# Kernel tuning notes

Measured on AMD Instinct MI355X. Metric: run time of the kernel, lower is better.

The kernel has to match this reference:

```python
import jax, jax.numpy as jnp
import numpy as np

N, IN_DIM, HID, OUT, NH = 512, 256, 256, 256, 4
HD = OUT // NH  # head_dim = 64
EPS = 1e-5


def _mlp(x, w1, b1, w2, b2):
    return jax.nn.relu(x @ w1 + b1) @ w2 + b2


def setup_inputs() -> dict:
    key = jax.random.key(0)
    ks = jax.random.split(key, 32)

    def rn(k, shape, fan_in):
        return (jax.random.normal(k, shape, jnp.float32) / np.float32(np.sqrt(fan_in)))

    V = jax.random.normal(ks[0], (N, IN_DIM), jnp.float32)
    adj = jax.random.randint(ks[1], (N, N), 0, 2, jnp.int32)
    adj = adj.at[jnp.arange(N), jnp.arange(N)].set(1)  # self-edges: avoid all -inf rows
    prev_hidden = jax.random.normal(ks[2], (N, HID), jnp.float32)
    z = jnp.zeros
    return dict(
        V=V, adj=adj, prev_hidden=prev_hidden,
        W1=rn(ks[3], (IN_DIM, HID), IN_DIM),
        a_std0=rn(ks[4], (HID, 1), HID), a_std1=rn(ks[5], (HID, 1), HID),
        ce_w1=rn(ks[6], (2 * IN_DIM, HID), 2 * IN_DIM), ce_b1=z((HID,), jnp.float32),
        ce_w2=rn(ks[7], (HID, HD), HID), ce_b2=z((HD,), jnp.float32),
        a_c0=rn(ks[8], (HD, 1), HD), a_c1=rn(ks[9], (HD, 1), HD),
        te_w1=rn(ks[10], (IN_DIM + HID, HID), IN_DIM + HID), te_b1=z((HID,), jnp.float32),
        te_w2=rn(ks[11], (HID, HD), HID), te_b2=z((HD,), jnp.float32),
        a_t0=rn(ks[12], (HD, 1), HD), a_t1=rn(ks[13], (HD, 1), HD),
        co_w1=rn(ks[14], (3 * IN_DIM, HID), 3 * IN_DIM), co_b1=z((HID,), jnp.float32),
        co_w2=rn(ks[15], (HID, HD), HID), co_b2=z((HD,), jnp.float32),
        a_co0=rn(ks[16], (HD, 1), HD), a_co1=rn(ks[17], (HD, 1), HD),
        W2=rn(ks[18], (HID + 2 * HD + 1, OUT), HID + 2 * HD + 1),
        Wo=rn(ks[19], (OUT, OUT), OUT), bo=z((OUT,), jnp.float32),
        ln_g=jnp.ones((OUT,), jnp.float32), ln_b=z((OUT,), jnp.float32),
    )


def reference(V, adj, prev_hidden, W1, a_std0, a_std1,
              ce_w1, ce_b1, ce_w2, ce_b2, a_c0, a_c1,
              te_w1, te_b1, te_w2, te_b2, a_t0, a_t1,
              co_w1, co_b1, co_w2, co_b2, a_co0, a_co1,
              W2, Wo, bo, ln_g, ln_b):
    ninf = -jnp.inf

    # ---- standard GAT branch -> H1: (N, HID) ----
    Wh1 = V @ W1
    s1 = Wh1 @ a_std0 + (Wh1 @ a_std1).T                      # (N, N)
    s1 = jnp.where(adj == 0, ninf, s1)
    H1 = jax.nn.softmax(s1, axis=1) @ Wh1

    # ---- causal branch: all ordered pairs i!=j, global softmax -> H2: (N, HD) ----
    pair = jnp.concatenate([jnp.broadcast_to(V[:, None, :], (N, N, IN_DIM)),
                            jnp.broadcast_to(V[None, :, :], (N, N, IN_DIM))], axis=-1)
    cf = _mlp(pair, ce_w1, ce_b1, ce_w2, ce_b2)               # (N, N, HD)
    cs = (cf @ (a_c0 + a_c1))[..., 0]                         # (N, N)
    cs = jnp.where(jnp.eye(N, dtype=bool), ninf, cs)          # exclude i==j pairs
    ca = jax.nn.softmax(cs.reshape(-1)).reshape(N, N, 1)
    H2 = jnp.broadcast_to((ca * cf).sum((0, 1)), (N, HD))

    # ---- temporal branch: (N,1) scores broadcast against causal mask -> running mean ----
    tf = _mlp(jnp.concatenate([V, prev_hidden], axis=-1), te_w1, te_b1, te_w2, te_b2)  # (N, HD)
    ts = tf @ (a_t0 + a_t1)                                   # (N, 1)
    cmask = jnp.triu(jnp.ones((N, N), bool), 1)
    tsb = jnp.where(cmask, ninf, jnp.broadcast_to(ts, (N, N)))
    H3 = jax.nn.softmax(tsb, axis=1) @ tf                     # (N, HD)

    # ---- coop branch: first two neighbors by index; size-1 softmax; buggy pad -> (N,1) ----
    order = jnp.argsort((1 - adj).astype(jnp.int32), axis=1, stable=True)  # adj==1 first, index order
    nb = V[order[:, :2]]                                      # (N, 2, IN_DIM)
    valid = ((adj == 1).sum(axis=1) >= 2)
    nb = jnp.where(valid[:, None, None], nb, jnp.zeros_like(nb))
    ci = jnp.concatenate([V, nb[:, 0], nb[:, 1]], axis=-1)    # (N, 3*IN_DIM)
    cf4 = _mlp(ci, co_w1, co_b1, co_w2, co_b2)                # (N, HD)
    ca4 = jax.nn.softmax(cf4 @ (a_co0 + a_co1), axis=1)       # (N,1): softmax over size-1 -> ones
    h4vec = (ca4.T @ cf4)[0]                                  # (HD,)
    # original: squeeze(-2)->(HD,), dim==1 -> unsqueeze(-1)->(HD,1), zero-pad rows to N
    H4 = jnp.zeros((N, 1), V.dtype).at[:HD, 0].set(h4vec)

    # ---- combine, lazy W2, proj, LN, ELU (dropout identity in eval) ----
    Hc = jnp.concatenate([H1, H2, H3, H4], axis=-1) @ W2      # (N, OUT)
    out = Hc @ Wo + bo
    mu = out.mean(-1, keepdims=True)
    var = ((out - mu) ** 2).mean(-1, keepdims=True)
    out = (out - mu) / jnp.sqrt(var + EPS) * ln_g + ln_b
    return jax.nn.elu(out)
```

## Files before the change

kernel.cpp:

```cpp
#include <hip/hip_runtime.h>
#include <math.h>

#define NN 512
#define HD 64
#define EPSV 1e-5f

struct GD {
  const float *A, *A2, *A3, *A4;
  const int* I;
  const float *B, *bias;
  float* C;
  int M, K, Nn, mode, act;
};

#define GEMM_SMEM (8704 + 17408 + 2176)
#define MEGA_SMEM 38656

__device__ __forceinline__ void gemm_body(char* smem, const GD& d, int bx, int by) {
  float (*At)[34] = (float (*)[34])smem;
  float (*Bs)[68] = (float (*)[68])(smem + 8704);
  char* extra = smem + 8704 + 17408;
  int* nbl = (int*)extra;
  float* wscl = (float*)extra;
  float* rowsuml = wscl + 512;

  const int t = threadIdx.x;
  const int tx = t & 15, ty = t >> 4;
  const int rowbase = by * 32, colbase = bx * 64;
  const int K = d.K, Nn = d.Nn, mode = d.mode, M = d.M;
  if (rowbase >= M) return;

  if (mode == 2) {
    int wave = t >> 6, lane = t & 63;
    for (int rr = wave; rr < 32; rr += 4) {
      int row = rowbase + rr;
      int n0 = -1, n1 = -1, cnt = 0;
      for (int c = 0; c < 8; ++c) {
        unsigned long long mm = __ballot(d.I[row * NN + c * 64 + lane] != 0);
        cnt += (int)__popcll(mm);
        if (n0 < 0 && mm) { n0 = c * 64 + (int)__builtin_ctzll(mm); mm &= mm - 1; }
        if (n1 < 0 && mm) { n1 = c * 64 + (int)__builtin_ctzll(mm); }
      }
      if (lane == 0) { nbl[rr * 3] = n0; nbl[rr * 3 + 1] = n1; nbl[rr * 3 + 2] = (cnt >= 2); }
    }
    __syncthreads();
  } else if (mode == 4) {
    wscl[t] = d.A2[t];
    wscl[256 + t] = d.A2[256 + t];
    __syncthreads();
  }

  float4 aR[2], bR[4];
  float rs0 = 0.f, rs1 = 0.f;

  auto loadA = [&](int k0) {
#pragma unroll
    for (int j = 0; j < 2; ++j) {
      int idx = t + j * 256;
      int r = idx >> 4, c0 = (idx & 15) * 4;
      int row = rowbase + r, gk = k0 + c0;
      float4 v4 = make_float4(0.f, 0.f, 0.f, 0.f);
      if (mode == 0) {
        if (row < M && gk < K) v4 = *(const float4*)&d.A[(size_t)row * K + gk];
      } else if (mode == 1) {
        if (gk < 256) v4 = *(const float4*)&d.A[row * 256 + gk];
        else v4 = *(const float4*)&d.A2[row * 256 + gk - 256];
      } else if (mode == 2) {
        int seg = gk >> 8;
        int src = (seg == 0) ? row : (nbl[r * 3 + 2] ? nbl[r * 3 + seg - 1] : -1);
        if (src >= 0) v4 = *(const float4*)&d.A[src * 256 + (gk & 255)];
      } else if (mode == 3) {
        if (gk + 3 < 256) v4 = *(const float4*)&d.A[row * 256 + gk];
        else if (gk >= 256 && gk + 3 < 320) v4 = *(const float4*)&d.A2[gk - 256];
        else if (gk >= 320 && gk + 3 < 384) v4 = *(const float4*)&d.A3[row * 64 + gk - 320];
        else if (gk == 384) v4.x = (row < 64) ? d.A4[row] : 0.f;
      } else {
        int4 a4 = *(const int4*)&d.I[row * NN + gk];
        v4.x = a4.x ? wscl[gk + 0] : 0.f;
        v4.y = a4.y ? wscl[gk + 1] : 0.f;
        v4.z = a4.z ? wscl[gk + 2] : 0.f;
        v4.w = a4.w ? wscl[gk + 3] : 0.f;
        float ss = v4.x + v4.y + v4.z + v4.w;
        if (j == 0) rs0 += ss; else rs1 += ss;
      }
      aR[j] = v4;
    }
  };
  auto loadB = [&](int k0) {
#pragma unroll
    for (int j = 0; j < 4; ++j) {
      int idx = t + j * 256;
      int r = idx >> 4, c0 = (idx & 15) * 4;
      int gk = k0 + r;
      float4 v4 = make_float4(0.f, 0.f, 0.f, 0.f);
      if (gk < K) v4 = *(const float4*)&d.B[(size_t)gk * Nn + colbase + c0];
      bR[j] = v4;
    }
  };
  auto stos = [&]() {
#pragma unroll
    for (int j = 0; j < 2; ++j) {
      int idx = t + j * 256;
      int r = idx >> 4, c0 = (idx & 15) * 4;
      At[c0 + 0][r] = aR[j].x;
      At[c0 + 1][r] = aR[j].y;
      At[c0 + 2][r] = aR[j].z;
      At[c0 + 3][r] = aR[j].w;
    }
#pragma unroll
    for (int j = 0; j < 4; ++j) {
      int idx = t + j * 256;
      int r = idx >> 4, c0 = (idx & 15) * 4;
      *(float4*)&Bs[r][c0] = bR[j];
    }
  };

  float4 acc0 = make_float4(0.f, 0.f, 0.f, 0.f);
  float4 acc1 = make_float4(0.f, 0.f, 0.f, 0.f);

  int iters = (K + 63) >> 6;
  loadA(0); loadB(0);
  for (int it = 0; it < iters; ++it) {
    stos();
    __syncthreads();
    if (it + 1 < iters) { loadA((it + 1) << 6); loadB((it + 1) << 6); }
#pragma unroll 8
    for (int kk = 0; kk < 64; ++kk) {
      float2 a = *(const float2*)&At[kk][ty * 2];
      float4 b = *(const float4*)&Bs[kk][tx * 4];
      acc0.x += a.x * b.x; acc0.y += a.x * b.y; acc0.z += a.x * b.z; acc0.w += a.x * b.w;
      acc1.x += a.y * b.x; acc1.y += a.y * b.y; acc1.z += a.y * b.z; acc1.w += a.y * b.w;
    }
    __syncthreads();
  }

  if (mode == 4) {
    float a0 = rs0, a1 = rs1;
#pragma unroll
    for (int off = 8; off; off >>= 1) {
      a0 += __shfl_xor(a0, off, 16);
      a1 += __shfl_xor(a1, off, 16);
    }
    if ((t & 15) == 0) { rowsuml[t >> 4] = a0; rowsuml[16 + (t >> 4)] = a1; }
    __syncthreads();
  }

  int col = colbase + tx * 4;
  float4 bv = make_float4(0.f, 0.f, 0.f, 0.f);
  if (d.bias) bv = *(const float4*)&d.bias[col];
  int row0 = rowbase + ty * 2;
  float4 o0, o1;
  o0.x = acc0.x + bv.x; o0.y = acc0.y + bv.y; o0.z = acc0.z + bv.z; o0.w = acc0.w + bv.w;
  o1.x = acc1.x + bv.x; o1.y = acc1.y + bv.y; o1.z = acc1.z + bv.z; o1.w = acc1.w + bv.w;
  if (d.act) {
    o0.x = fmaxf(o0.x, 0.f); o0.y = fmaxf(o0.y, 0.f); o0.z = fmaxf(o0.z, 0.f); o0.w = fmaxf(o0.w, 0.f);
    o1.x = fmaxf(o1.x, 0.f); o1.y = fmaxf(o1.y, 0.f); o1.z = fmaxf(o1.z, 0.f); o1.w = fmaxf(o1.w, 0.f);
  }
  if (mode == 4) {
    float s0 = 1.f / rowsuml[ty * 2], s1 = 1.f / rowsuml[ty * 2 + 1];
    o0.x *= s0; o0.y *= s0; o0.z *= s0; o0.w *= s0;
    o1.x *= s1; o1.y *= s1; o1.z *= s1; o1.w *= s1;
  }
  if (row0 < M)     *(float4*)&d.C[(size_t)row0 * Nn + col] = o0;
  if (row0 + 1 < M) *(float4*)&d.C[(size_t)(row0 + 1) * Nn + col] = o1;
}

__device__ void wsc_body(char* smem, const float* W1, const float* a_std1,
                         const float* V, float* expwsc, int grp) {
  float* asl = (float*)smem;
  float* ul  = asl + 256;
  int t = threadIdx.x;
  asl[t] = a_std1[t];
  __syncthreads();
  {
    float s = 0.f;
    const float* wr = W1 + t * 256;
    for (int h = 0; h < 256; h += 4) {
      float4 w4 = *(const float4*)&wr[h];
      float4 a4 = *(const float4*)&asl[h];
      s += w4.x * a4.x + w4.y * a4.y + w4.z * a4.z + w4.w * a4.w;
    }
    ul[t] = s;
  }
  __syncthreads();
  int wave = t >> 6, lane = t & 63;
  float4 u4 = *(const float4*)&ul[lane * 4];
  int j0 = grp * 128;
  for (int j = j0 + wave; j < j0 + 128; j += 4) {
    float4 v4 = *(const float4*)&V[j * 256 + lane * 4];
    float s = v4.x * u4.x + v4.y * u4.y + v4.z * u4.z + v4.w * u4.w;
#pragma unroll
    for (int off = 32; off; off >>= 1) s += __shfl_xor(s, off, 64);
    if (lane == 0) expwsc[j] = __expf(s);
  }
}

struct GD7 { GD d[7]; };
__global__ __launch_bounds__(256) void gemm7_k(GD7 ds) {
  __shared__ __align__(16) char smem[GEMM_SMEM];
  int z = blockIdx.z;
  if (z == 6) {
    if (blockIdx.y != 0) return;
    wsc_body(smem, ds.d[6].A, ds.d[6].A2, ds.d[6].A3, ds.d[6].C, blockIdx.x);
    return;
  }
  gemm_body(smem, ds.d[z], blockIdx.x, blockIdx.y);
}
__global__ __launch_bounds__(256) void gemm1_k(GD d) {
  __shared__ __align__(16) char smem[GEMM_SMEM];
  gemm_body(smem, d, blockIdx.x, blockIdx.y);
}

__device__ void pair_body(char* smem,
    const float* __restrict__ P, const float* __restrict__ Q,
    const float* __restrict__ b1, const float* __restrict__ ce_w2,
    const float* __restrict__ a_c0, const float* __restrict__ a_c1,
    float* __restrict__ mpart, float* __restrict__ dpart,
    float* __restrict__ spart, int byy, int bxx) {
  float* Pl  = (float*)smem;
  float* Ql  = Pl + 16 * 260;
  float* el  = Ql + 16 * 260;
  float* wcl = el + 16 * 20;
  float* red = wcl + 256;
  float* sk  = red + 256;
  float* sbl = sk + 256;
  int t = threadIdx.x;

  if (t < 64) red[t] = a_c0[t] + a_c1[t];
  __syncthreads();
  {
    float s = 0.f;
    const float* w2r = ce_w2 + t * 64;
#pragma unroll 8
    for (int h = 0; h < 64; ++h) s += w2r[h] * red[h];
    wcl[t] = s;
  }
  int i0 = byy * 16, j0 = bxx * 16;
  for (int e = t; e < 1024; e += 256) {
    int r = e >> 6, c4 = (e & 63) * 4;
    float4 bb = *(const float4*)&b1[c4];
    float4 pv = *(const float4*)&P[(i0 + r) * 256 + c4];
    pv.x += bb.x; pv.y += bb.y; pv.z += bb.z; pv.w += bb.w;
    *(float4*)&Pl[r * 260 + c4] = pv;
    *(float4*)&Ql[r * 260 + c4] = *(const float4*)&Q[(j0 + r) * 256 + c4];
  }
  __syncthreads();

  int a = t >> 4, b = t & 15;
  const float* pr = &Pl[a * 260];
  const float* qr = &Ql[b * 260];
  float4 c4a = make_float4(0.f, 0.f, 0.f, 0.f);
#pragma unroll 8
  for (int k4 = 0; k4 < 64; ++k4) {
    float4 w = *(const float4*)&wcl[k4 * 4];
    float4 p = *(const float4*)&pr[k4 * 4];
    float4 q = *(const float4*)&qr[k4 * 4];
    c4a.x += fmaxf(p.x + q.x, 0.f) * w.x;
    c4a.y += fmaxf(p.y + q.y, 0.f) * w.y;
    c4a.z += fmaxf(p.z + q.z, 0.f) * w.z;
    c4a.w += fmaxf(p.w + q.w, 0.f) * w.w;
  }
  float s = c4a.x + c4a.y + c4a.z + c4a.w;
  if (i0 + a == j0 + b) s = -INFINITY;
  red[t] = s; __syncthreads();
  for (int ss = 128; ss; ss >>= 1) { if (t < ss) red[t] = fmaxf(red[t], red[t + ss]); __syncthreads(); }
  float mb = red[0];
  __syncthreads();
  float e = __expf(s - mb);
  el[a * 20 + b] = e;
  red[t] = e; __syncthreads();
  for (int ss = 128; ss; ss >>= 1) { if (t < ss) red[t] += red[t + ss]; __syncthreads(); }
  float db = red[0];
  __syncthreads();

  float qv[16];
#pragma unroll
  for (int j = 0; j < 16; ++j) qv[j] = Ql[j * 260 + t];
  float rk = 0.f;
#pragma unroll 4
  for (int i = 0; i < 16; ++i) {
    float pv = Pl[i * 260 + t];
    const float* erow = &el[i * 20];
#pragma unroll
    for (int j4 = 0; j4 < 4; ++j4) {
      float4 e4 = *(const float4*)&erow[j4 * 4];
      rk += e4.x * fmaxf(pv + qv[j4 * 4 + 0], 0.f);
      rk += e4.y * fmaxf(pv + qv[j4 * 4 + 1], 0.f);
      rk += e4.z * fmaxf(pv + qv[j4 * 4 + 2], 0.f);
      rk += e4.w * fmaxf(pv + qv[j4 * 4 + 3], 0.f);
    }
  }
  sk[t] = rk;
  __syncthreads();
  {
    int h = t & 63, q = t >> 6;
    float s2 = 0.f;
    for (int k = q * 64; k < q * 64 + 64; ++k) s2 += sk[k] * ce_w2[k * 64 + h];
    sbl[q * 64 + h] = s2;
  }
  __syncthreads();
  int blk = byy * 32 + bxx;
  if (t < 64) spart[blk * 64 + t] = sbl[t] + sbl[64 + t] + sbl[128 + t] + sbl[192 + t];
  if (t == 0) { mpart[blk] = mb; dpart[blk] = db; }
}

struct MegaArgs {
  const float *P, *Q, *b1, *ce_w2, *a_c0, *a_c1;
  float *mpart, *dpart, *spart;
  GD gH1, gTf, gCf;
};

__global__ __launch_bounds__(256) void mega_k(MegaArgs a) {
  __shared__ __align__(16) char smem[MEGA_SMEM];
  int b = blockIdx.x;
  if (b < 64) {
    gemm_body(smem, a.gH1, b & 3, b >> 2);
  } else if (b < 80) {
    gemm_body(smem, a.gTf, 0, b - 64);
  } else if (b < 96) {
    gemm_body(smem, a.gCf, 0, b - 80);
  } else {
    int p = b - 96;
    pair_body(smem, a.P, a.Q, a.b1, a.ce_w2, a.a_c0, a.a_c1,
              a.mpart, a.dpart, a.spart, p >> 5, p & 31);
  }
}

__global__ __launch_bounds__(1024) void mini_k(
    const float* __restrict__ mpart, const float* __restrict__ dpart,
    const float* __restrict__ spart, const float* __restrict__ ce_b2,
    float* __restrict__ H2row,
    const float* __restrict__ tf, float* __restrict__ H3,
    const float* __restrict__ cf4, float* __restrict__ h4vec) {
  __shared__ float A[1024];
  __shared__ float Bsh[1024];
  __shared__ float segsum[16][65];
  int b = blockIdx.x, t = threadIdx.x;
  if (b == 0) {
    float mv = mpart[t];
    A[t] = mv; __syncthreads();
    for (int s = 512; s; s >>= 1) { if (t < s) A[t] = fmaxf(A[t], A[t + s]); __syncthreads(); }
    float M = A[0];
    __syncthreads();
    float e = __expf(mv - M);
    Bsh[t] = e;
    A[t] = e * dpart[t];
    __syncthreads();
    for (int s = 512; s; s >>= 1) { if (t < s) A[t] += A[t + s]; __syncthreads(); }
    float D = A[0];
    __syncthreads();
    int h = t & 63, g = t >> 6;
    float s2 = 0.f;
    for (int b2 = g * 64; b2 < g * 64 + 64; ++b2) s2 += Bsh[b2] * spart[b2 * 64 + h];
    A[t] = s2;
    __syncthreads();
    for (int p = 8; p; p >>= 1) { if (g < p) A[g * 64 + h] += A[(g + p) * 64 + h]; __syncthreads(); }
    if (t < 64) H2row[t] = A[t] / D + ce_b2[t];
  } else if (b == 1) {
    int h = t & 63, g = t >> 6;
    float vals[32];
    float run = 0.f;
#pragma unroll
    for (int r = 0; r < 32; ++r) { run += tf[(g * 32 + r) * 64 + h]; vals[r] = run; }
    segsum[g][h] = run;
    __syncthreads();
    float off = 0.f;
    for (int gg = 0; gg < g; ++gg) off += segsum[gg][h];
#pragma unroll
    for (int r = 0; r < 32; ++r) {
      int i = g * 32 + r;
      H3[i * 64 + h] = (vals[r] + off) / (float)(i + 1);
    }
  } else {
    int h = t & 63, g = t >> 6;
    float s = 0.f;
    for (int r = 0; r < 32; ++r) s += cf4[(g * 32 + r) * 64 + h];
    A[g * 64 + h] = s;
    __syncthreads();
    for (int p = 8; p; p >>= 1) { if (g < p) A[g * 64 + h] += A[(g + p) * 64 + h]; __syncthreads(); }
    if (t < 64) h4vec[t] = A[t];
  }
}

__global__ void ln_elu_kernel(const float* __restrict__ X, const float* __restrict__ g,
                              const float* __restrict__ b, float* __restrict__ out) {
  __shared__ float red[256];
  int i = blockIdx.x, tid = threadIdx.x;
  float x = X[i * 256 + tid];
  red[tid] = x; __syncthreads();
  for (int s = 128; s; s >>= 1) { if (tid < s) red[tid] += red[tid + s]; __syncthreads(); }
  float mu = red[0] * (1.f / 256.f);
  __syncthreads();
  float d = x - mu;
  red[tid] = d * d; __syncthreads();
  for (int s = 128; s; s >>= 1) { if (tid < s) red[tid] += red[tid + s]; __syncthreads(); }
  float var = red[0] * (1.f / 256.f);
  float y = d / sqrtf(var + EPSV) * g[tid] + b[tid];
  out[i * 256 + tid] = (y > 0.f) ? y : (expf(y) - 1.f);
}

static GD mkgd(const float* A, const float* A2, const float* A3, const float* A4,
               const int* I, const float* B, const float* bias, float* C,
               int M, int K, int Nn, int mode, int act) {
  GD g{A, A2, A3, A4, I, B, bias, C, M, K, Nn, mode, act};
  return g;
}

extern "C" void kernel_launch(void* const* d_in, const int* in_sizes, int n_in,
                              void* d_out, int out_size, void* d_ws, size_t ws_size,
                              hipStream_t stream) {
  const float* V      = (const float*)d_in[0];
  const int*   adj    = (const int*)  d_in[1];
  const float* ph     = (const float*)d_in[2];
  const float* W1     = (const float*)d_in[3];
  const float* a_std1 = (const float*)d_in[5];
  const float* ce_w1  = (const float*)d_in[6];
  const float* ce_b1  = (const float*)d_in[7];
  const float* ce_w2  = (const float*)d_in[8];
  const float* ce_b2  = (const float*)d_in[9];
  const float* a_c0   = (const float*)d_in[10];
  const float* a_c1   = (const float*)d_in[11];
  const float* te_w1  = (const float*)d_in[12];
  const float* te_b1  = (const float*)d_in[13];
  const float* te_w2  = (const float*)d_in[14];
  const float* te_b2  = (const float*)d_in[15];
  const float* co_w1  = (const float*)d_in[18];
  const float* co_b1  = (const float*)d_in[19];
  const float* co_w2  = (const float*)d_in[20];
  const float* co_b2  = (const float*)d_in[21];
  const float* W2     = (const float*)d_in[24];
  const float* Wo     = (const float*)d_in[25];
  const float* bo     = (const float*)d_in[26];
  const float* ln_g   = (const float*)d_in[27];
  const float* ln_b   = (const float*)d_in[28];
  float* out = (float*)d_out;

  float* ws = (float*)d_ws;
  size_t off = 0;
  auto alloc = [&](size_t n) { float* p = ws + off; off += (n + 15) & ~(size_t)15; return p; };

  float* Wh1    = alloc(512 * 256);
  float* Pb     = alloc(512 * 256);
  float* Qb     = alloc(512 * 256);
  float* tfh    = alloc(512 * 256);
  float* cf4h   = alloc(512 * 256);
  float* H1     = alloc(512 * 256);
  float* Wfused = alloc(385 * 256);
  float* T2     = alloc(512 * 256);
  float* tf     = alloc(512 * 64);
  float* cf4    = alloc(512 * 64);
  float* H3     = alloc(512 * 64);
  float* spart  = alloc(1024 * 64);
  float* mpart  = alloc(1024);
  float* dpart  = alloc(1024);
  float* expwsc = alloc(512);
  float* H2row  = alloc(64);
  float* h4vec  = alloc(64);
  (void)ws_size; (void)in_sizes; (void)n_in; (void)out_size;

  GD7 sA;
  sA.d[0] = mkgd(V, 0, 0, 0, 0, W1, 0, Wh1, 512, 256, 256, 0, 0);
  sA.d[1] = mkgd(V, 0, 0, 0, 0, ce_w1, 0, Pb, 512, 256, 256, 0, 0);
  sA.d[2] = mkgd(V, 0, 0, 0, 0, ce_w1 + 256 * 256, 0, Qb, 512, 256, 256, 0, 0);
  sA.d[3] = mkgd(V, ph, 0, 0, 0, te_w1, te_b1, tfh, 512, 512, 256, 1, 1);
  sA.d[4] = mkgd(V, 0, 0, 0, adj, co_w1, co_b1, cf4h, 512, 768, 256, 2, 1);
  sA.d[5] = mkgd(W2, 0, 0, 0, 0, Wo, 0, Wfused, 385, 256, 256, 0, 0);
  sA.d[6] = mkgd(W1, a_std1, V, 0, 0, 0, 0, expwsc, 512, 256, 1, 6, 0);
  gemm7_k<<<dim3(4, 16, 7), 256, 0, stream>>>(sA);

  MegaArgs ma;
  ma.P = Pb; ma.Q = Qb; ma.b1 = ce_b1; ma.ce_w2 = ce_w2;
  ma.a_c0 = a_c0; ma.a_c1 = a_c1;
  ma.mpart = mpart; ma.dpart = dpart; ma.spart = spart;
  ma.gH1 = mkgd(0, expwsc, 0, 0, adj, Wh1, 0, H1, 512, 512, 256, 4, 0);
  ma.gTf = mkgd(tfh, 0, 0, 0, 0, te_w2, te_b2, tf, 512, 256, 64, 0, 0);
  ma.gCf = mkgd(cf4h, 0, 0, 0, 0, co_w2, co_b2, cf4, 512, 256, 64, 0, 0);
  mega_k<<<1120, 256, 0, stream>>>(ma);

  mini_k<<<3, 1024, 0, stream>>>(mpart, dpart, spart, ce_b2, H2row, tf, H3, cf4, h4vec);

  GD gF = mkgd(H1, H2row, H3, h4vec, 0, Wfused, bo, T2, 512, 385, 256, 3, 0);
  gemm1_k<<<dim3(4, 16), 256, 0, stream>>>(gF);

  ln_elu_kernel<<<512, 256, 0, stream>>>(T2, ln_g, ln_b, out);
}
```

Baseline: 201.8 us.

## Use split-bf16 MFMA (3-pass) for the tiled GEMM instead of FP32 FMAs

Replaces the scalar FP32 inner product in the shared GEMM body with MFMA 16x16x32 bf16 instructions. Each float operand is split into high and low bf16 halves, and three MFMA passes (hh, hl, lh) approximate FP32 accuracy. The shared-memory layout changes to bf16 high/low tiles, with B transposed. The epilogue is remapped to the MFMA output layout, which writes scalars instead of float4. The aim is to cut ALU time in the matmuls, at the cost of extra split work, scalar stores, and slightly lower precision.

```diff
diff --git a/kernel.cpp b/kernel.cpp
--- a/kernel.cpp
+++ b/kernel.cpp
@@ -4,6 +4,11 @@
 #define NN 512
 #define HD 64
 #define EPSV 1e-5f
+
+typedef unsigned short u16;
+typedef short s4v __attribute__((ext_vector_type(4)));
+typedef short s8v __attribute__((ext_vector_type(8)));
+typedef float f4v __attribute__((ext_vector_type(4)));
 
 struct GD {
   const float *A, *A2, *A3, *A4;
@@ -13,19 +18,27 @@
   int M, K, Nn, mode, act;
 };
 
-#define GEMM_SMEM (8704 + 17408 + 2176)
+#define GEMM_SMEM 28800
 #define MEGA_SMEM 38656
 
+__device__ __forceinline__ void split_bf16(float x, u16& h, u16& l) {
+  unsigned xb = __float_as_uint(x);
+  float hf = __uint_as_float(xb & 0xffff0000u);
+  h = (u16)(xb >> 16);
+  l = (u16)(__float_as_uint(x - hf) >> 16);
+}
+
 __device__ __forceinline__ void gemm_body(char* smem, const GD& d, int bx, int by) {
-  float (*At)[34] = (float (*)[34])smem;
-  float (*Bs)[68] = (float (*)[68])(smem + 8704);
-  char* extra = smem + 8704 + 17408;
+  u16 (*Ah)[72] = (u16(*)[72])smem;
+  u16 (*Al)[72] = (u16(*)[72])(smem + 4608);
+  u16 (*Bh)[68] = (u16(*)[68])(smem + 9216);
+  u16 (*Bl)[68] = (u16(*)[68])(smem + 9216 + 8704);
+  char* extra = smem + 26624;
   int* nbl = (int*)extra;
   float* wscl = (float*)extra;
   float* rowsuml = wscl + 512;
 
   const int t = threadIdx.x;
-  const int tx = t & 15, ty = t >> 4;
   const int rowbase = by * 32, colbase = bx * 64;
   const int K = d.K, Nn = d.Nn, mode = d.mode, M = d.M;
   if (rowbase >= M) return;
@@ -102,21 +115,34 @@
     for (int j = 0; j < 2; ++j) {
       int idx = t + j * 256;
       int r = idx >> 4, c0 = (idx & 15) * 4;
-      At[c0 + 0][r] = aR[j].x;
-      At[c0 + 1][r] = aR[j].y;
-      At[c0 + 2][r] = aR[j].z;
-      At[c0 + 3][r] = aR[j].w;
+      float v[4] = {aR[j].x, aR[j].y, aR[j].z, aR[j].w};
+      u16 h[4], l[4];
+#pragma unroll
+      for (int e = 0; e < 4; ++e) split_bf16(v[e], h[e], l[e]);
+      *(short4*)&Ah[r][c0] = make_short4(h[0], h[1], h[2], h[3]);
+      *(short4*)&Al[r][c0] = make_short4(l[0], l[1], l[2], l[3]);
     }
 #pragma unroll
     for (int j = 0; j < 4; ++j) {
       int idx = t + j * 256;
       int r = idx >> 4, c0 = (idx & 15) * 4;
-      *(float4*)&Bs[r][c0] = bR[j];
+      float v[4] = {bR[j].x, bR[j].y, bR[j].z, bR[j].w};
+#pragma unroll
+      for (int e = 0; e < 4; ++e) {
+        u16 h, l;
+        split_bf16(v[e], h, l);
+        Bh[c0 + e][r] = h;
+        Bl[c0 + e][r] = l;
+      }
     }
   };
 
-  float4 acc0 = make_float4(0.f, 0.f, 0.f, 0.f);
-  float4 acc1 = make_float4(0.f, 0.f, 0.f, 0.f);
+  f4v acc0 = {0.f, 0.f, 0.f, 0.f};
+  f4v acc1 = {0.f, 0.f, 0.f, 0.f};
+
+  const int w4 = t >> 6;
+  const int lrow = t & 15;
+  const int lk = ((t & 63) >> 4) * 8;
 
   int iters = (K + 63) >> 6;
   loadA(0); loadB(0);
@@ -124,12 +150,31 @@
     stos();
     __syncthreads();
     if (it + 1 < iters) { loadA((it + 1) << 6); loadB((it + 1) << 6); }
-#pragma unroll 8
-    for (int kk = 0; kk < 64; ++kk) {
-      float2 a = *(const float2*)&At[kk][ty * 2];
-      float4 b = *(const float4*)&Bs[kk][tx * 4];
-      acc0.x += a.x * b.x; acc0.y += a.x * b.y; acc0.z += a.x * b.z; acc0.w += a.x * b.w;
-      acc1.x += a.y * b.x; acc1.y += a.y * b.y; acc1.z += a.y * b.z; acc1.w += a.y * b.w;
+    const u16* bhrow = Bh[w4 * 16 + lrow];
+    const u16* blrow = Bl[w4 * 16 + lrow];
+#pragma unroll
+    for (int ks = 0; ks < 2; ++ks) {
+      int ko = ks * 32 + lk;
+      s4v bh_0 = *(const s4v*)&bhrow[ko];
+      s4v bh_1 = *(const s4v*)&bhrow[ko + 4];
+      s4v bl_0 = *(const s4v*)&blrow[ko];
+      s4v bl_1 = *(const s4v*)&blrow[ko + 4];
+      s8v bh = __builtin_shufflevector(bh_0, bh_1, 0, 1, 2, 3, 4, 5, 6, 7);
+      s8v bl = __builtin_shufflevector(bl_0, bl_1, 0, 1, 2, 3, 4, 5, 6, 7);
+      {
+        s8v ah = *(const s8v*)&Ah[lrow][ko];
+        s8v al = *(const s8v*)&Al[lrow][ko];
+        acc0 = __builtin_amdgcn_mfma_f32_16x16x32_bf16(ah, bh, acc0, 0, 0, 0);
+        acc0 = __builtin_amdgcn_mfma_f32_16x16x32_bf16(ah, bl, acc0, 0, 0, 0);
+        acc0 = __builtin_amdgcn_mfma_f32_16x16x32_bf16(al, bh, acc0, 0, 0, 0);
+      }
+      {
+        s8v ah = *(const s8v*)&Ah[16 + lrow][ko];
+        s8v al = *(const s8v*)&Al[16 + lrow][ko];
+        acc1 = __builtin_amdgcn_mfma_f32_16x16x32_bf16(ah, bh, acc1, 0, 0, 0);
+        acc1 = __builtin_amdgcn_mfma_f32_16x16x32_bf16(ah, bl, acc1, 0, 0, 0);
+        acc1 = __builtin_amdgcn_mfma_f32_16x16x32_bf16(al, bh, acc1, 0, 0, 0);
+      }
     }
     __syncthreads();
   }
@@ -145,24 +190,22 @@
     __syncthreads();
   }
 
-  int col = colbase + tx * 4;
-  float4 bv = make_float4(0.f, 0.f, 0.f, 0.f);
-  if (d.bias) bv = *(const float4*)&d.bias[col];
-  int row0 = rowbase + ty * 2;
-  float4 o0, o1;
-  o0.x = acc0.x + bv.x; o0.y = acc0.y + bv.y; o0.z = acc0.z + bv.z; o0.w = acc0.w + bv.w;
-  o1.x = acc1.x + bv.x; o1.y = acc1.y + bv.y; o1.z = acc1.z + bv.z; o1.w = acc1.w + bv.w;
-  if (d.act) {
-    o0.x = fmaxf(o0.x, 0.f); o0.y = fmaxf(o0.y, 0.f); o0.z = fmaxf(o0.z, 0.f); o0.w = fmaxf(o0.w, 0.f);
-    o1.x = fmaxf(o1.x, 0.f); o1.y = fmaxf(o1.y, 0.f); o1.z = fmaxf(o1.z, 0.f); o1.w = fmaxf(o1.w, 0.f);
-  }
-  if (mode == 4) {
-    float s0 = 1.f / rowsuml[ty * 2], s1 = 1.f / rowsuml[ty * 2 + 1];
-    o0.x *= s0; o0.y *= s0; o0.z *= s0; o0.w *= s0;
-    o1.x *= s1; o1.y *= s1; o1.z *= s1; o1.w *= s1;
-  }
-  if (row0 < M)     *(float4*)&d.C[(size_t)row0 * Nn + col] = o0;
-  if (row0 + 1 < M) *(float4*)&d.C[(size_t)(row0 + 1) * Nn + col] = o1;
+  int col = colbase + w4 * 16 + lrow;
+  float bvs = d.bias ? d.bias[col] : 0.f;
+  int qrow = ((t & 63) >> 4) * 4;
+#pragma unroll
+  for (int m = 0; m < 2; ++m) {
+#pragma unroll
+    for (int q = 0; q < 4; ++q) {
+      int lr = m * 16 + qrow + q;
+      int row = rowbase + lr;
+      if (row >= M) continue;
+      float o = (m ? acc1[q] : acc0[q]) + bvs;
+      if (d.act) o = fmaxf(o, 0.f);
+      if (mode == 4) o *= (1.f / rowsuml[lr]);
+      d.C[(size_t)row * Nn + col] = o;
+    }
+  }
 }
 
 __device__ void wsc_body(char* smem, const float* W1, const float* a_std1,
```

New measurement: 193.7 us. 1.04x faster.
